# Kernel optimization log

Measured on AMD Instinct MI355X. Metric: run time of the kernel, lower is better.

The kernel has to match this reference:

```python
import jax, jax.numpy as jnp
import numpy as np

B, N, D, H = 4, 2048, 512, 8
HEAD = D // H
TEMP = 8.0


def setup_inputs() -> dict:
    key = jax.random.key(0)
    k1, k2, k3, k4 = jax.random.split(key, 4)
    return {
        "keys": jax.random.normal(k1, (B, N, D), dtype=jnp.float32),
        "queries": jax.random.normal(k2, (B, N, D), dtype=jnp.float32),
        "values": jax.random.normal(k3, (B, N, D), dtype=jnp.float32),
        "W_comb": jax.random.normal(k4, (D, D), dtype=jnp.float32) * (1.0 / np.sqrt(D)),
        "b_comb": jnp.zeros((D,), dtype=jnp.float32),
    }


def reference(keys, queries, values, W_comb, b_comb):
    b, nk, d = keys.shape
    nq = queries.shape[1]
    h, hd = H, HEAD
    # split heads: (b, n, d) -> (b, n, h, hd)
    k = keys.reshape(b, nk, h, hd)
    q = queries.reshape(b, nq, h, hd)
    v = values.reshape(b, nk, h, hd)
    # scaled dot-product attention per head
    logits = jnp.einsum("bqhd,bkhd->bhqk", q, k) / TEMP  # (b, h, nq, nk)
    w = jax.nn.softmax(logits, axis=-1)
    out = jnp.einsum("bhqk,bkhd->bqhd", w, v).reshape(b, nq, d)
    # head_combine: Linear with bias (torch: x @ W.T + b)
    return out @ W_comb.T + b_comb
```

## Files before the change

kernel.cpp:

```cpp
#include <hip/hip_runtime.h>

#define B_ 4
#define N_ 2048
#define D_ 512
#define H_ 8

typedef __attribute__((ext_vector_type(8))) short bf16x8;
typedef __attribute__((ext_vector_type(4))) short bf16x4;
typedef __attribute__((ext_vector_type(4))) float f32x4;

__device__ __forceinline__ unsigned short f32_to_bf16(float f) {
  unsigned int u = __float_as_uint(f);
  u += 0x7FFFu + ((u >> 16) & 1u);
  return (unsigned short)(u >> 16);
}

__device__ __forceinline__ unsigned int pack2_bf16(float a, float b) {
#if __has_builtin(__builtin_amdgcn_cvt_pk_bf16_f32)
  typedef __attribute__((ext_vector_type(2))) __bf16 bf16v2;
  bf16v2 r = __builtin_amdgcn_cvt_pk_bf16_f32(a, b);
  return *(unsigned int*)&r;
#else
  return (unsigned int)f32_to_bf16(a) | ((unsigned int)f32_to_bf16(b) << 16);
#endif
}

__device__ __forceinline__ float fast_exp2(float x) {
#if __has_builtin(__builtin_amdgcn_exp2f)
  return __builtin_amdgcn_exp2f(x);
#else
  return exp2f(x);
#endif
}

__device__ __forceinline__ f32x4 mfma16(bf16x4 a, bf16x4 b, f32x4 c) {
#if __has_builtin(__builtin_amdgcn_mfma_f32_16x16x16_bf16)
  return __builtin_amdgcn_mfma_f32_16x16x16_bf16(a, b, c, 0, 0, 0);
#else
  return __builtin_amdgcn_mfma_f32_16x16x16bf16_1k(a, b, c, 0, 0, 0);
#endif
}

__device__ __forceinline__ int lds_sw(int row, int chunk) {
  return row * 64 + ((chunk ^ (row & 7)) * 8);
}

__global__ __launch_bounds__(256) void convert_kernel(
    const float* __restrict__ Kf, const float* __restrict__ Qf,
    const float* __restrict__ Vf, const float* __restrict__ Wf,
    unsigned short* __restrict__ Qb, unsigned short* __restrict__ Kb,
    unsigned short* __restrict__ Wb, unsigned short* __restrict__ Vt) {
  __shared__ float tile[64 * 72];
  const int tid = threadIdx.x;
  if (blockIdx.x < 1024) {
    const float qs = 0.125f * 1.4426950408889634f;
    int gid = blockIdx.x * 256 + tid;
    const float4* Q4 = (const float4*)Qf;
    const float4* K4 = (const float4*)Kf;
    for (int i = gid; i < (B_ * N_ * D_) / 4; i += 262144) {
      float4 q = Q4[i];
      ((uint2*)Qb)[i] = make_uint2(pack2_bf16(q.x * qs, q.y * qs),
                                   pack2_bf16(q.z * qs, q.w * qs));
      float4 k = K4[i];
      ((uint2*)Kb)[i] = make_uint2(pack2_bf16(k.x, k.y), pack2_bf16(k.z, k.w));
    }
    if (gid < (D_ * D_) / 4) {
      float4 w = ((const float4*)Wf)[gid];
      ((uint2*)Wb)[gid] = make_uint2(pack2_bf16(w.x, w.y), pack2_bf16(w.z, w.w));
    }
  } else {
    int bid = blockIdx.x - 1024;
    int nt = bid & 31, bh = bid >> 5;
    int b = bh >> 3, h = bh & 7;
    int n0 = nt * 64;
#pragma unroll
    for (int i = 0; i < 4; ++i) {
      int idx = i * 256 + tid;
      int r = idx >> 4, c = idx & 15;
      *(float4*)&tile[r * 72 + c * 4] =
          *(const float4*)(Vf + (size_t)(b * N_ + n0 + r) * D_ + h * 64 + c * 4);
    }
    __syncthreads();
    int d = tid >> 2, c = tid & 3;
    unsigned int o[8];
#pragma unroll
    for (int j = 0; j < 8; ++j)
      o[j] = pack2_bf16(tile[(c * 16 + 2 * j) * 72 + d],
                        tile[(c * 16 + 2 * j + 1) * 72 + d]);
    unsigned short* dst = Vt + ((size_t)bh * 64 + d) * N_ + n0 + c * 16;
    *(bf16x8*)dst = *(bf16x8*)&o[0];
    *(bf16x8*)(dst + 8) = *(bf16x8*)&o[4];
  }
}

union AttnLDS {
  struct { unsigned short K[2][64 * 64]; unsigned short V[2][64 * 64]; } loop;
  struct { float O[2][64 * 68]; float l[2][64]; } red;
};

__global__ __launch_bounds__(256, 2) void attn_kernel(
    const unsigned short* __restrict__ Qb, const unsigned short* __restrict__ Kb,
    const unsigned short* __restrict__ Vt, unsigned short* __restrict__ Ob) {
  __shared__ AttnLDS lds;

  const int tid = threadIdx.x;
  const int w = tid >> 6;
  const int lane = tid & 63;
  const int lr = lane & 15;
  const int lq = lane >> 4;

  const int bh = blockIdx.y;
  const int qb = blockIdx.x * 64;
  const size_t slab = (size_t)(bh >> 3) * N_ * D_ + (size_t)(bh & 7) * 64;
  const unsigned short* kbase = Kb + slab;
  const unsigned short* vtbase = Vt + (size_t)bh * 64 * N_;

  bf16x8 qa[4][2];
#pragma unroll
  for (int qt = 0; qt < 4; ++qt) {
    const unsigned short* qrow = Qb + slab + (size_t)(qb + qt * 16 + lr) * D_;
    qa[qt][0] = *(const bf16x8*)(qrow + 8 * lq);
    qa[qt][1] = *(const bf16x8*)(qrow + 32 + 8 * lq);
  }

  f32x4 O[4][4];
#pragma unroll
  for (int i = 0; i < 4; ++i)
#pragma unroll
    for (int j = 0; j < 4; ++j) O[i][j] = (f32x4){0.f, 0.f, 0.f, 0.f};
  float l_part[4] = {0.f, 0.f, 0.f, 0.f};

  const int st_r = tid >> 3;
  const int st_c = tid & 7;

  {
    const unsigned short* ksrc = kbase + (size_t)st_r * D_ + st_c * 8;
    bf16x8 a = *(const bf16x8*)ksrc;
    bf16x8 b = *(const bf16x8*)(ksrc + (size_t)32 * D_);
    const unsigned short* vsrc = vtbase + (size_t)st_r * N_ + st_c * 8;
    bf16x8 c = *(const bf16x8*)vsrc;
    bf16x8 d = *(const bf16x8*)(vsrc + (size_t)32 * N_);
    *(bf16x8*)&lds.loop.K[0][lds_sw(st_r, st_c)] = a;
    *(bf16x8*)&lds.loop.K[0][lds_sw(st_r + 32, st_c)] = b;
    *(bf16x8*)&lds.loop.V[0][lds_sw(st_r, st_c)] = c;
    *(bf16x8*)&lds.loop.V[0][lds_sw(st_r + 32, st_c)] = d;
  }

  for (int kt = 0; kt < 32; ++kt) {
    const int p = kt & 1;
    __syncthreads();

    bf16x8 nk0, nk1, nv0, nv1;
    const bool more = (kt + 1) < 32;
    if (more) {
      const int kb1 = (kt + 1) * 64;
      const unsigned short* ksrc = kbase + (size_t)(kb1 + st_r) * D_ + st_c * 8;
      nk0 = *(const bf16x8*)ksrc;
      nk1 = *(const bf16x8*)(ksrc + (size_t)32 * D_);
      const unsigned short* vsrc = vtbase + (size_t)st_r * N_ + kb1 + st_c * 8;
      nv0 = *(const bf16x8*)vsrc;
      nv1 = *(const bf16x8*)(vsrc + (size_t)32 * N_);
    }

    bf16x8 kf0 = *(const bf16x8*)&lds.loop.K[p][lds_sw(w * 16 + lr, lq)];
    bf16x8 kf1 = *(const bf16x8*)&lds.loop.K[p][lds_sw(w * 16 + lr, lq + 4)];

    f32x4 S[4];
#pragma unroll
    for (int qt = 0; qt < 4; ++qt) {
      S[qt] = __builtin_amdgcn_mfma_f32_16x16x32_bf16(
          kf0, qa[qt][0], (f32x4){0.f, 0.f, 0.f, 0.f}, 0, 0, 0);
      S[qt] = __builtin_amdgcn_mfma_f32_16x16x32_bf16(kf1, qa[qt][1], S[qt],
                                                      0, 0, 0);
    }

    bf16x4 pf[4];
#pragma unroll
    for (int qt = 0; qt < 4; ++qt) {
      float p0 = fast_exp2(S[qt][0]);
      float p1 = fast_exp2(S[qt][1]);
      float p2 = fast_exp2(S[qt][2]);
      float p3 = fast_exp2(S[qt][3]);
      l_part[qt] += (p0 + p1) + (p2 + p3);
      uint2 packed = make_uint2(pack2_bf16(p0, p1), pack2_bf16(p2, p3));
      pf[qt] = *(bf16x4*)&packed;
    }

#pragma unroll
    for (int dt = 0; dt < 4; ++dt) {
      const int row = dt * 16 + lr;
      const int scol = w * 16 + 4 * lq;
      const int chunk = scol >> 3;
      const int off = scol & 7;
      bf16x4 vf = *(const bf16x4*)&lds.loop.V[p][lds_sw(row, chunk) + off];
#pragma unroll
      for (int qt = 0; qt < 4; ++qt)
        O[dt][qt] = mfma16(vf, pf[qt], O[dt][qt]);
    }

    if (more) {
      *(bf16x8*)&lds.loop.K[1 - p][lds_sw(st_r, st_c)] = nk0;
      *(bf16x8*)&lds.loop.K[1 - p][lds_sw(st_r + 32, st_c)] = nk1;
      *(bf16x8*)&lds.loop.V[1 - p][lds_sw(st_r, st_c)] = nv0;
      *(bf16x8*)&lds.loop.V[1 - p][lds_sw(st_r + 32, st_c)] = nv1;
    }
  }

#pragma unroll
  for (int qt = 0; qt < 4; ++qt) {
    l_part[qt] += __shfl_xor(l_part[qt], 16);
    l_part[qt] += __shfl_xor(l_part[qt], 32);
  }

  __syncthreads();

  if (w >= 2) {
    const int g = w - 2;
#pragma unroll
    for (int dt = 0; dt < 4; ++dt)
#pragma unroll
      for (int qt = 0; qt < 4; ++qt)
        *(f32x4*)&lds.red.O[g][(qt * 16 + lr) * 68 + dt * 16 + lq * 4] =
            O[dt][qt];
    if (lq == 0) {
#pragma unroll
      for (int qt = 0; qt < 4; ++qt)
        lds.red.l[g][qt * 16 + lr] = l_part[qt];
    }
  }
  __syncthreads();

  if (w < 2) {
    const int g = w;
#pragma unroll
    for (int dt = 0; dt < 4; ++dt)
#pragma unroll
      for (int qt = 0; qt < 4; ++qt) {
        f32x4 t = *(const f32x4*)&lds.red
                      .O[g][(qt * 16 + lr) * 68 + dt * 16 + lq * 4];
        O[dt][qt][0] += t[0]; O[dt][qt][1] += t[1];
        O[dt][qt][2] += t[2]; O[dt][qt][3] += t[3];
      }
#pragma unroll
    for (int qt = 0; qt < 4; ++qt)
      l_part[qt] += lds.red.l[g][qt * 16 + lr];
  }
  __syncthreads();

  if (w == 1) {
#pragma unroll
    for (int dt = 0; dt < 4; ++dt)
#pragma unroll
      for (int qt = 0; qt < 4; ++qt)
        *(f32x4*)&lds.red.O[0][(qt * 16 + lr) * 68 + dt * 16 + lq * 4] =
            O[dt][qt];
    if (lq == 0) {
#pragma unroll
      for (int qt = 0; qt < 4; ++qt)
        lds.red.l[0][qt * 16 + lr] = l_part[qt];
    }
  }
  __syncthreads();

  unsigned short* S16 = (unsigned short*)&lds.red.O[1][0];
  if (w == 0) {
    float linv[4];
#pragma unroll
    for (int qt = 0; qt < 4; ++qt) {
      float lt = l_part[qt] + lds.red.l[0][qt * 16 + lr];
      linv[qt] = 1.0f / lt;
    }
#pragma unroll
    for (int dt = 0; dt < 4; ++dt)
#pragma unroll
      for (int qt = 0; qt < 4; ++qt) {
        f32x4 t = *(const f32x4*)&lds.red
                      .O[0][(qt * 16 + lr) * 68 + dt * 16 + lq * 4];
        float v0 = (O[dt][qt][0] + t[0]) * linv[qt];
        float v1 = (O[dt][qt][1] + t[1]) * linv[qt];
        float v2 = (O[dt][qt][2] + t[2]) * linv[qt];
        float v3 = (O[dt][qt][3] + t[3]) * linv[qt];
        uint2 packed = make_uint2(pack2_bf16(v0, v1), pack2_bf16(v2, v3));
        *(bf16x4*)&S16[(qt * 16 + lr) * 72 + dt * 16 + lq * 4] =
            *(bf16x4*)&packed;
      }
  }
  __syncthreads();

  {
    const int row = tid >> 2, ch = tid & 3;
    unsigned short* dst = Ob + slab + (size_t)(qb + row) * D_ + ch * 16;
    *(bf16x8*)dst = *(const bf16x8*)&S16[row * 72 + ch * 16];
    *(bf16x8*)(dst + 8) = *(const bf16x8*)&S16[row * 72 + ch * 16 + 8];
  }
}

__global__ __launch_bounds__(256) void gemm_kernel(
    const unsigned short* __restrict__ A, const unsigned short* __restrict__ Wb,
    const float* __restrict__ bias, float* __restrict__ out) {
  __shared__ unsigned short A_lds[2][64 * 72];
  __shared__ unsigned short W_lds[2][64 * 72];

  const int tid = threadIdx.x;
  const int w = tid >> 6;
  const int lane = tid & 63;
  const int lr = lane & 15;
  const int lq = lane >> 4;

  const int cb = blockIdx.x * 64;
  const int mb = blockIdx.y * 64;

  const int dc = (tid & 7) * 8;
  const int r0 = tid >> 3;

  f32x4 acc[4];
#pragma unroll
  for (int i = 0; i < 4; ++i) acc[i] = (f32x4){0.f, 0.f, 0.f, 0.f};

  {
    *(bf16x8*)&A_lds[0][r0 * 72 + dc] =
        *(const bf16x8*)(A + (size_t)(mb + r0) * D_ + dc);
    *(bf16x8*)&A_lds[0][(r0 + 32) * 72 + dc] =
        *(const bf16x8*)(A + (size_t)(mb + r0 + 32) * D_ + dc);
    *(bf16x8*)&W_lds[0][r0 * 72 + dc] =
        *(const bf16x8*)(Wb + (size_t)(cb + r0) * D_ + dc);
    *(bf16x8*)&W_lds[0][(r0 + 32) * 72 + dc] =
        *(const bf16x8*)(Wb + (size_t)(cb + r0 + 32) * D_ + dc);
  }

  for (int kt = 0; kt < 8; ++kt) {
    const int p = kt & 1;
    __syncthreads();

    bf16x8 na0, na1, nw0, nw1;
    const bool more = (kt + 1) < 8;
    if (more) {
      const int k1 = (kt + 1) * 64;
      na0 = *(const bf16x8*)(A + (size_t)(mb + r0) * D_ + k1 + dc);
      na1 = *(const bf16x8*)(A + (size_t)(mb + r0 + 32) * D_ + k1 + dc);
      nw0 = *(const bf16x8*)(Wb + (size_t)(cb + r0) * D_ + k1 + dc);
      nw1 = *(const bf16x8*)(Wb + (size_t)(cb + r0 + 32) * D_ + k1 + dc);
    }

    bf16x8 a0 = *(const bf16x8*)&A_lds[p][(w * 16 + lr) * 72 + 8 * lq];
    bf16x8 a1 = *(const bf16x8*)&A_lds[p][(w * 16 + lr) * 72 + 32 + 8 * lq];
#pragma unroll
    for (int nt = 0; nt < 4; ++nt) {
      bf16x8 b0 = *(const bf16x8*)&W_lds[p][(nt * 16 + lr) * 72 + 8 * lq];
      bf16x8 b1 = *(const bf16x8*)&W_lds[p][(nt * 16 + lr) * 72 + 32 + 8 * lq];
      acc[nt] = __builtin_amdgcn_mfma_f32_16x16x32_bf16(a0, b0, acc[nt], 0, 0, 0);
      acc[nt] = __builtin_amdgcn_mfma_f32_16x16x32_bf16(a1, b1, acc[nt], 0, 0, 0);
    }

    if (more) {
      *(bf16x8*)&A_lds[1 - p][r0 * 72 + dc] = na0;
      *(bf16x8*)&A_lds[1 - p][(r0 + 32) * 72 + dc] = na1;
      *(bf16x8*)&W_lds[1 - p][r0 * 72 + dc] = nw0;
      *(bf16x8*)&W_lds[1 - p][(r0 + 32) * 72 + dc] = nw1;
    }
  }

#pragma unroll
  for (int nt = 0; nt < 4; ++nt) {
    float bc = bias[cb + nt * 16 + lr];
#pragma unroll
    for (int rr = 0; rr < 4; ++rr) {
      int row = mb + w * 16 + lq * 4 + rr;
      out[(size_t)row * D_ + cb + nt * 16 + lr] = acc[nt][rr] + bc;
    }
  }
}

extern "C" void kernel_launch(void* const* d_in, const int* in_sizes, int n_in,
                              void* d_out, int out_size, void* d_ws,
                              size_t ws_size, hipStream_t stream) {
  (void)in_sizes; (void)n_in; (void)out_size; (void)ws_size;
  const float* keys    = (const float*)d_in[0];
  const float* queries = (const float*)d_in[1];
  const float* values  = (const float*)d_in[2];
  const float* W       = (const float*)d_in[3];
  const float* bias    = (const float*)d_in[4];
  float* out = (float*)d_out;

  char* ws = (char*)d_ws;
  unsigned short* Qb = (unsigned short*)(ws);
  unsigned short* Kb = (unsigned short*)(ws + 8388608);
  unsigned short* Vt = (unsigned short*)(ws + 16777216);
  unsigned short* Wb = (unsigned short*)(ws + 25165824);
  unsigned short* Ab = (unsigned short*)(ws + 25690112);

  convert_kernel<<<2048, 256, 0, stream>>>(keys, queries, values, W,
                                           Qb, Kb, Wb, Vt);

  attn_kernel<<<dim3(N_ / 64, B_ * H_), 256, 0, stream>>>(Qb, Kb, Vt, Ab);

  gemm_kernel<<<dim3(D_ / 64, (B_ * N_) / 64), 256, 0, stream>>>(Ab, Wb, bias,
                                                                 out);
}
```

Baseline: 185.9 us.

## Load V fragments directly from global, shrink attention LDS, raise occupancy to 3

The attention kernel stops staging V through LDS. Each lane now loads its transposed-V MFMA operand straight from global memory, double-buffered in registers across a 2x-unrolled loop. K stays in LDS with a padded, non-swizzled layout, and the cross-wave output reduction runs in two column halves so the LDS union fits in smaller buffers. Together these cut LDS use per block so launch bounds can request 3 blocks per SIMD, meant to hide latency better. The trade-off is uncoalesced 8-byte global V loads, more register pressure, and extra barriers in the epilogue.

```diff
diff --git a/kernel.cpp b/kernel.cpp
--- a/kernel.cpp
+++ b/kernel.cpp
@@ -39,10 +39,6 @@
 #else
   return __builtin_amdgcn_mfma_f32_16x16x16bf16_1k(a, b, c, 0, 0, 0);
 #endif
-}
-
-__device__ __forceinline__ int lds_sw(int row, int chunk) {
-  return row * 64 + ((chunk ^ (row & 7)) * 8);
 }
 
 __global__ __launch_bounds__(256) void convert_kernel(
@@ -94,11 +90,11 @@
 }
 
 union AttnLDS {
-  struct { unsigned short K[2][64 * 64]; unsigned short V[2][64 * 64]; } loop;
-  struct { float O[2][64 * 68]; float l[2][64]; } red;
+  unsigned short K[2][64 * 72];
+  float R[2][64 * 36];
 };
 
-__global__ __launch_bounds__(256, 2) void attn_kernel(
+__global__ __launch_bounds__(256, 3) void attn_kernel(
     const unsigned short* __restrict__ Qb, const unsigned short* __restrict__ Kb,
     const unsigned short* __restrict__ Vt, unsigned short* __restrict__ Ob) {
   __shared__ AttnLDS lds;
@@ -123,6 +119,11 @@
     qa[qt][1] = *(const bf16x8*)(qrow + 32 + 8 * lq);
   }
 
+  const unsigned short* vp[4];
+#pragma unroll
+  for (int dt = 0; dt < 4; ++dt)
+    vp[dt] = vtbase + (size_t)(dt * 16 + lr) * N_ + w * 16 + 4 * lq;
+
   f32x4 O[4][4];
 #pragma unroll
   for (int i = 0; i < 4; ++i)
@@ -137,33 +138,31 @@
     const unsigned short* ksrc = kbase + (size_t)st_r * D_ + st_c * 8;
     bf16x8 a = *(const bf16x8*)ksrc;
     bf16x8 b = *(const bf16x8*)(ksrc + (size_t)32 * D_);
-    const unsigned short* vsrc = vtbase + (size_t)st_r * N_ + st_c * 8;
-    bf16x8 c = *(const bf16x8*)vsrc;
-    bf16x8 d = *(const bf16x8*)(vsrc + (size_t)32 * N_);
-    *(bf16x8*)&lds.loop.K[0][lds_sw(st_r, st_c)] = a;
-    *(bf16x8*)&lds.loop.K[0][lds_sw(st_r + 32, st_c)] = b;
-    *(bf16x8*)&lds.loop.V[0][lds_sw(st_r, st_c)] = c;
-    *(bf16x8*)&lds.loop.V[0][lds_sw(st_r + 32, st_c)] = d;
-  }
-
-  for (int kt = 0; kt < 32; ++kt) {
+    *(bf16x8*)&lds.K[0][st_r * 72 + st_c * 8] = a;
+    *(bf16x8*)&lds.K[0][(st_r + 32) * 72 + st_c * 8] = b;
+  }
+  bf16x4 vA[4], vB[4];
+#pragma unroll
+  for (int dt = 0; dt < 4; ++dt) vA[dt] = *(const bf16x4*)vp[dt];
+
+  auto body = [&](int kt, bf16x4* vcur, bf16x4* vnext) {
     const int p = kt & 1;
     __syncthreads();
 
-    bf16x8 nk0, nk1, nv0, nv1;
+    bf16x8 nk0, nk1;
     const bool more = (kt + 1) < 32;
     if (more) {
       const int kb1 = (kt + 1) * 64;
       const unsigned short* ksrc = kbase + (size_t)(kb1 + st_r) * D_ + st_c * 8;
       nk0 = *(const bf16x8*)ksrc;
       nk1 = *(const bf16x8*)(ksrc + (size_t)32 * D_);
-      const unsigned short* vsrc = vtbase + (size_t)st_r * N_ + kb1 + st_c * 8;
-      nv0 = *(const bf16x8*)vsrc;
-      nv1 = *(const bf16x8*)(vsrc + (size_t)32 * N_);
-    }
-
-    bf16x8 kf0 = *(const bf16x8*)&lds.loop.K[p][lds_sw(w * 16 + lr, lq)];
-    bf16x8 kf1 = *(const bf16x8*)&lds.loop.K[p][lds_sw(w * 16 + lr, lq + 4)];
+#pragma unroll
+      for (int dt = 0; dt < 4; ++dt)
+        vnext[dt] = *(const bf16x4*)(vp[dt] + kb1);
+    }
+
+    bf16x8 kf0 = *(const bf16x8*)&lds.K[p][(w * 16 + lr) * 72 + 8 * lq];
+    bf16x8 kf1 = *(const bf16x8*)&lds.K[p][(w * 16 + lr) * 72 + 32 + 8 * lq];
 
     f32x4 S[4];
 #pragma unroll
@@ -187,23 +186,20 @@
     }
 
 #pragma unroll
-    for (int dt = 0; dt < 4; ++dt) {
-      const int row = dt * 16 + lr;
-      const int scol = w * 16 + 4 * lq;
-      const int chunk = scol >> 3;
-      const int off = scol & 7;
-      bf16x4 vf = *(const bf16x4*)&lds.loop.V[p][lds_sw(row, chunk) + off];
+    for (int dt = 0; dt < 4; ++dt)
 #pragma unroll
       for (int qt = 0; qt < 4; ++qt)
-        O[dt][qt] = mfma16(vf, pf[qt], O[dt][qt]);
-    }
+        O[dt][qt] = mfma16(vcur[dt], pf[qt], O[dt][qt]);
 
     if (more) {
-      *(bf16x8*)&lds.loop.K[1 - p][lds_sw(st_r, st_c)] = nk0;
-      *(bf16x8*)&lds.loop.K[1 - p][lds_sw(st_r + 32, st_c)] = nk1;
-      *(bf16x8*)&lds.loop.V[1 - p][lds_sw(st_r, st_c)] = nv0;
-      *(bf16x8*)&lds.loop.V[1 - p][lds_sw(st_r + 32, st_c)] = nv1;
-    }
+      *(bf16x8*)&lds.K[1 - p][st_r * 72 + st_c * 8] = nk0;
+      *(bf16x8*)&lds.K[1 - p][(st_r + 32) * 72 + st_c * 8] = nk1;
+    }
+  };
+
+  for (int k2 = 0; k2 < 16; ++k2) {
+    body(2 * k2, vA, vB);
+    body(2 * k2 + 1, vB, vA);
   }
 
 #pragma unroll
@@ -212,86 +208,87 @@
     l_part[qt] += __shfl_xor(l_part[qt], 32);
   }
 
-  __syncthreads();
-
-  if (w >= 2) {
-    const int g = w - 2;
-#pragma unroll
-    for (int dt = 0; dt < 4; ++dt)
-#pragma unroll
-      for (int qt = 0; qt < 4; ++qt)
-        *(f32x4*)&lds.red.O[g][(qt * 16 + lr) * 68 + dt * 16 + lq * 4] =
-            O[dt][qt];
-    if (lq == 0) {
-#pragma unroll
-      for (int qt = 0; qt < 4; ++qt)
-        lds.red.l[g][qt * 16 + lr] = l_part[qt];
-    }
-  }
-  __syncthreads();
-
-  if (w < 2) {
-    const int g = w;
-#pragma unroll
-    for (int dt = 0; dt < 4; ++dt)
-#pragma unroll
-      for (int qt = 0; qt < 4; ++qt) {
-        f32x4 t = *(const f32x4*)&lds.red
-                      .O[g][(qt * 16 + lr) * 68 + dt * 16 + lq * 4];
-        O[dt][qt][0] += t[0]; O[dt][qt][1] += t[1];
-        O[dt][qt][2] += t[2]; O[dt][qt][3] += t[3];
+  float linv[4];
+  unsigned short* SR = (unsigned short*)&lds.R[1][0];
+#pragma unroll
+  for (int c = 0; c < 2; ++c) {
+    __syncthreads();
+    if (w >= 2) {
+      float* Rg = (w == 2) ? &lds.R[0][0] : &lds.R[1][0];
+#pragma unroll
+      for (int dh = 0; dh < 2; ++dh)
+#pragma unroll
+        for (int qt = 0; qt < 4; ++qt)
+          *(f32x4*)&Rg[(qt * 16 + lr) * 36 + dh * 16 + lq * 4] =
+              O[c * 2 + dh][qt];
+      if (c == 0 && lq == 0) {
+#pragma unroll
+        for (int qt = 0; qt < 4; ++qt)
+          Rg[(qt * 16 + lr) * 36 + 32] = l_part[qt];
       }
-#pragma unroll
-    for (int qt = 0; qt < 4; ++qt)
-      l_part[qt] += lds.red.l[g][qt * 16 + lr];
-  }
-  __syncthreads();
-
-  if (w == 1) {
-#pragma unroll
-    for (int dt = 0; dt < 4; ++dt)
-#pragma unroll
-      for (int qt = 0; qt < 4; ++qt)
-        *(f32x4*)&lds.red.O[0][(qt * 16 + lr) * 68 + dt * 16 + lq * 4] =
-            O[dt][qt];
-    if (lq == 0) {
-#pragma unroll
-      for (int qt = 0; qt < 4; ++qt)
-        lds.red.l[0][qt * 16 + lr] = l_part[qt];
-    }
-  }
-  __syncthreads();
-
-  unsigned short* S16 = (unsigned short*)&lds.red.O[1][0];
-  if (w == 0) {
-    float linv[4];
-#pragma unroll
-    for (int qt = 0; qt < 4; ++qt) {
-      float lt = l_part[qt] + lds.red.l[0][qt * 16 + lr];
-      linv[qt] = 1.0f / lt;
-    }
-#pragma unroll
-    for (int dt = 0; dt < 4; ++dt)
-#pragma unroll
-      for (int qt = 0; qt < 4; ++qt) {
-        f32x4 t = *(const f32x4*)&lds.red
-                      .O[0][(qt * 16 + lr) * 68 + dt * 16 + lq * 4];
-        float v0 = (O[dt][qt][0] + t[0]) * linv[qt];
-        float v1 = (O[dt][qt][1] + t[1]) * linv[qt];
-        float v2 = (O[dt][qt][2] + t[2]) * linv[qt];
-        float v3 = (O[dt][qt][3] + t[3]) * linv[qt];
-        uint2 packed = make_uint2(pack2_bf16(v0, v1), pack2_bf16(v2, v3));
-        *(bf16x4*)&S16[(qt * 16 + lr) * 72 + dt * 16 + lq * 4] =
-            *(bf16x4*)&packed;
+    }
+    __syncthreads();
+    if (w < 2) {
+      float* Rg = (w == 0) ? &lds.R[0][0] : &lds.R[1][0];
+#pragma unroll
+      for (int dh = 0; dh < 2; ++dh)
+#pragma unroll
+        for (int qt = 0; qt < 4; ++qt) {
+          f32x4 t = *(const f32x4*)&Rg[(qt * 16 + lr) * 36 + dh * 16 + lq * 4];
+          O[c * 2 + dh][qt][0] += t[0]; O[c * 2 + dh][qt][1] += t[1];
+          O[c * 2 + dh][qt][2] += t[2]; O[c * 2 + dh][qt][3] += t[3];
+        }
+      if (c == 0) {
+#pragma unroll
+        for (int qt = 0; qt < 4; ++qt)
+          l_part[qt] += Rg[(qt * 16 + lr) * 36 + 32];
       }
-  }
-  __syncthreads();
-
-  {
-    const int row = tid >> 2, ch = tid & 3;
-    unsigned short* dst = Ob + slab + (size_t)(qb + row) * D_ + ch * 16;
-    *(bf16x8*)dst = *(const bf16x8*)&S16[row * 72 + ch * 16];
-    *(bf16x8*)(dst + 8) = *(const bf16x8*)&S16[row * 72 + ch * 16 + 8];
+    }
+    __syncthreads();
+    if (w == 1) {
+#pragma unroll
+      for (int dh = 0; dh < 2; ++dh)
+#pragma unroll
+        for (int qt = 0; qt < 4; ++qt)
+          *(f32x4*)&lds.R[0][(qt * 16 + lr) * 36 + dh * 16 + lq * 4] =
+              O[c * 2 + dh][qt];
+      if (c == 0 && lq == 0) {
+#pragma unroll
+        for (int qt = 0; qt < 4; ++qt)
+          lds.R[0][(qt * 16 + lr) * 36 + 32] = l_part[qt];
+      }
+    }
+    __syncthreads();
+    if (w == 0) {
+      if (c == 0) {
+#pragma unroll
+        for (int qt = 0; qt < 4; ++qt) {
+          float lt = l_part[qt] + lds.R[0][(qt * 16 + lr) * 36 + 32];
+          linv[qt] = 1.0f / lt;
+        }
+      }
+#pragma unroll
+      for (int dh = 0; dh < 2; ++dh)
+#pragma unroll
+        for (int qt = 0; qt < 4; ++qt) {
+          f32x4 t = *(const f32x4*)&lds
+                        .R[0][(qt * 16 + lr) * 36 + dh * 16 + lq * 4];
+          float v0 = (O[c * 2 + dh][qt][0] + t[0]) * linv[qt];
+          float v1 = (O[c * 2 + dh][qt][1] + t[1]) * linv[qt];
+          float v2 = (O[c * 2 + dh][qt][2] + t[2]) * linv[qt];
+          float v3 = (O[c * 2 + dh][qt][3] + t[3]) * linv[qt];
+          uint2 packed = make_uint2(pack2_bf16(v0, v1), pack2_bf16(v2, v3));
+          *(bf16x4*)&SR[(qt * 16 + lr) * 32 + dh * 16 + lq * 4] =
+              *(bf16x4*)&packed;
+        }
+    }
+    __syncthreads();
+    {
+      const int row = tid >> 2, seg = tid & 3;
+      unsigned short* dst =
+          Ob + slab + (size_t)(qb + row) * D_ + c * 32 + seg * 8;
+      *(bf16x8*)dst = *(const bf16x8*)&SR[row * 32 + seg * 8];
+    }
   }
 }
 
```

Result: slower. 205.0 us (+10.3%).
